# Performance work log

Hardware: AMD Instinct MI355X
Metric: run time of the kernel (lower is better)

The kernel has to match this reference:

```python
import jax, jax.numpy as jnp
import numpy as np

B, S, D = 4, 4096, 1024
E, I = 8, 2048
CAPACITY = 2
K = max(1, int(S / E * CAPACITY))  # tokens per expert per batch element


def setup_inputs() -> dict:
    key = jax.random.key(0)
    k1, k2, k3, k4, k5 = jax.random.split(key, 5)
    x = jax.random.normal(k1, (B, S, D), dtype=jnp.float32)
    gate_w = jax.random.normal(k2, (D, E), dtype=jnp.float32) * 0.006
    Wg = jax.random.normal(k3, (E, D, I), dtype=jnp.float32) * 0.02
    Wu = jax.random.normal(k4, (E, D, I), dtype=jnp.float32) * 0.02
    Wd = jax.random.normal(k5, (E, I, D), dtype=jnp.float32) * 0.02
    return {"x": x, "gate_w": gate_w, "Wg": Wg, "Wu": Wu, "Wd": Wd}


def reference(x, gate_w, Wg, Wu, Wd):
    # Router: softmax over experts per token, then per-expert top-k tokens.
    logits = jnp.einsum('bsd,de->bse', x, gate_w)          # [B,S,E]
    affinity = jax.nn.softmax(logits, axis=-1)
    affinity_T = jnp.transpose(affinity, (0, 2, 1))        # [B,E,S]
    gating, index = jax.lax.top_k(affinity_T, K)           # [B,E,K]

    # Gather selected tokens for all experts at once: [B,E,K,D]
    b_idx = jnp.arange(x.shape[0])[:, None, None]
    x_sel = x[b_idx, index]

    # Per-expert SwiGLU MLP (grouped GEMMs over the expert axis).
    g = jnp.einsum('bekd,edi->beki', x_sel, Wg)
    u = jnp.einsum('bekd,edi->beki', x_sel, Wu)
    h = jax.nn.silu(g) * u
    out = jnp.einsum('beki,eid->bekd', h, Wd)              # [B,E,K,D]

    # Weighted scatter-add combine back to token positions.
    contrib = out * gating[..., None]
    x_out = jnp.zeros_like(x).at[b_idx, index].add(contrib)
    return x_out
```

## Files before the change

kernel.cpp:

```cpp
#include <hip/hip_runtime.h>

#define B_ 4
#define S_ 4096
#define D_ 1024
#define E_ 8
#define I_ 2048
#define K_ 1024

typedef __attribute__((ext_vector_type(8))) short short8;
typedef __attribute__((ext_vector_type(4))) float f32x4;

__device__ __forceinline__ short f2bf(float f) {
  union { float f; unsigned u; } v; v.f = f;
  unsigned r = v.u + 0x7FFFu + ((v.u >> 16) & 1u);
  return (short)(r >> 16);
}

__device__ __forceinline__ void gload16(const void* g, void* l) {
  __builtin_amdgcn_global_load_lds((const __attribute__((address_space(1))) unsigned int*)g,
                                   (__attribute__((address_space(3))) unsigned int*)l, 16, 0, 0);
}

__device__ __forceinline__ short8 rdswz(const short* ls, int row, int cb) {
  int byte = (row << 7) + (cb ^ ((row & 7) << 4));
  return *reinterpret_cast<const short8*>(reinterpret_cast<const char*>(ls) + byte);
}

__global__ __launch_bounds__(256) void router_kernel(const float* __restrict__ x,
                                                     const float* __restrict__ gw,
                                                     double* __restrict__ affD) {
  int wave = threadIdx.x >> 6, lane = threadIdx.x & 63;
  int tok = blockIdx.x * 4 + wave;
  int b = tok >> 12, s = tok & (S_ - 1);
  const float* xr = x + (size_t)tok * D_;
  double acc[E_];
#pragma unroll
  for (int e = 0; e < E_; ++e) acc[e] = 0.0;
#pragma unroll 4
  for (int r = 0; r < 16; ++r) {
    int d = r * 64 + lane;
    float xv = xr[d];
    const float4* g4 = reinterpret_cast<const float4*>(gw + (size_t)d * E_);
    float4 g0 = g4[0], g1 = g4[1];
    acc[0] += (double)xv * g0.x; acc[1] += (double)xv * g0.y;
    acc[2] += (double)xv * g0.z; acc[3] += (double)xv * g0.w;
    acc[4] += (double)xv * g1.x; acc[5] += (double)xv * g1.y;
    acc[6] += (double)xv * g1.z; acc[7] += (double)xv * g1.w;
  }
#pragma unroll
  for (int off = 32; off > 0; off >>= 1) {
#pragma unroll
    for (int e = 0; e < E_; ++e) acc[e] += __shfl_xor(acc[e], off, 64);
  }
  double m = acc[0];
#pragma unroll
  for (int e = 1; e < E_; ++e) m = acc[e] > m ? acc[e] : m;
  double den = 0.0, ex[E_];
#pragma unroll
  for (int e = 0; e < E_; ++e) { ex[e] = exp(acc[e] - m); den += ex[e]; }
  if (lane < E_)
    affD[((size_t)b * E_ + lane) * S_ + s] = ex[lane] / den;
}

__global__ __launch_bounds__(1024) void topk_select_kernel(const double* __restrict__ affD,
                                                           int* __restrict__ idxArr,
                                                           float* __restrict__ gateArr) {
  __shared__ unsigned hist[256];
  __shared__ unsigned s_digit;
  __shared__ int s_rem;
  __shared__ unsigned s_cnt;
  int be = blockIdx.x, tid = threadIdx.x;
  const double* a = affD + (size_t)be * S_;
  unsigned long long key[4];
  bool active[4];
#pragma unroll
  for (int c = 0; c < 4; ++c) {
    int i = tid + c * 1024;
    unsigned long long kb = (unsigned long long)__double_as_longlong(a[i]);
    key[c] = (kb & ~0xFFFULL) | (unsigned long long)(4095 - i);
    active[c] = true;
  }
  int remk = K_;
  unsigned long long prefix = 0;
  for (int pass = 0; pass < 8; ++pass) {
    int shift = 56 - pass * 8;
    if (tid < 256) hist[tid] = 0;
    __syncthreads();
#pragma unroll
    for (int c = 0; c < 4; ++c)
      if (active[c]) atomicAdd(&hist[(unsigned)((key[c] >> shift) & 0xFF)], 1u);
    __syncthreads();
    if (tid == 0) {
      unsigned cum = 0; int d = 255;
      for (; d > 0; --d) {
        unsigned h = hist[d];
        if (cum + h >= (unsigned)remk) break;
        cum += h;
      }
      s_digit = (unsigned)d;
      s_rem = remk - (int)cum;
    }
    __syncthreads();
    unsigned dg = s_digit; remk = s_rem;
    prefix |= ((unsigned long long)dg) << shift;
#pragma unroll
    for (int c = 0; c < 4; ++c)
      active[c] = active[c] && (((key[c] >> shift) & 0xFF) == dg);
    __syncthreads();
  }
  if (tid == 0) s_cnt = 0;
  __syncthreads();
#pragma unroll
  for (int c = 0; c < 4; ++c) {
    if (key[c] >= prefix) {
      unsigned slot = atomicAdd(&s_cnt, 1u);
      int i = 4095 - (int)(key[c] & 0xFFF);
      idxArr[(size_t)be * K_ + slot] = i;
      gateArr[(size_t)be * K_ + slot] = (float)a[i];
    }
  }
}

__global__ __launch_bounds__(256) void transpose_cvt_kernel(const float* __restrict__ in,
                                                            unsigned short* __restrict__ out,
                                                            int M, int N) {
  __shared__ float t[64][65];
  int e = blockIdx.y;
  int ntn = N >> 6;
  int tm = (blockIdx.x / ntn) << 6;
  int tn = (blockIdx.x % ntn) << 6;
  const float* src = in + (size_t)e * M * N;
  unsigned short* dst = out + (size_t)e * M * N;
  int tid = threadIdx.x;
#pragma unroll
  for (int it = 0; it < 4; ++it) {
    int f = it * 256 + tid;
    int r = f >> 4, c4 = (f & 15) << 2;
    float4 v = *reinterpret_cast<const float4*>(&src[(size_t)(tm + r) * N + tn + c4]);
    t[c4][r] = v.x; t[c4 + 1][r] = v.y; t[c4 + 2][r] = v.z; t[c4 + 3][r] = v.w;
  }
  __syncthreads();
#pragma unroll
  for (int it = 0; it < 4; ++it) {
    int f = it * 256 + tid;
    int rr = f >> 4, c4 = (f & 15) << 2;
    short4 o;
    o.x = f2bf(t[rr][c4]); o.y = f2bf(t[rr][c4 + 1]);
    o.z = f2bf(t[rr][c4 + 2]); o.w = f2bf(t[rr][c4 + 3]);
    *reinterpret_cast<short4*>(&dst[(size_t)(tn + rr) * M + tm + c4]) = o;
  }
}

__global__ __launch_bounds__(256) void gather_cvt_kernel(const float* __restrict__ x,
                                                         const int* __restrict__ idxArr,
                                                         unsigned short* __restrict__ Xsel) {
  int row = blockIdx.x * 4 + (threadIdx.x >> 6);
  int lane = threadIdx.x & 63;
  int b = row >> 13;
  int tok = idxArr[row];
  const float* src = x + ((size_t)b * S_ + tok) * D_;
  unsigned short* dst = Xsel + (size_t)row * D_;
#pragma unroll
  for (int it = 0; it < 4; ++it) {
    int d = it * 256 + lane * 4;
    float4 v = *reinterpret_cast<const float4*>(src + d);
    short4 o;
    o.x = f2bf(v.x); o.y = f2bf(v.y); o.z = f2bf(v.z); o.w = f2bf(v.w);
    *reinterpret_cast<short4*>(dst + d) = o;
  }
}

__global__ __launch_bounds__(256, 2) void mlp1_kernel(
    const unsigned short* __restrict__ Xsel, const unsigned short* __restrict__ WgT,
    const unsigned short* __restrict__ WuT, unsigned short* __restrict__ H, int kc) {
  int nwg = gridDim.x;
  int bid = (blockIdx.x & 7) * (nwg >> 3) + (blockIdx.x >> 3);
  int nt = bid & 15; bid >>= 4;
  int mt = bid & 3; bid >>= 2;
  int be = bid;
  int e = be & 7;

  __shared__ short lsA[128 * 64];
  __shared__ short lsBg[128 * 64];
  __shared__ short lsBu[128 * 64];

  int tid = threadIdx.x, w = tid >> 6, lane = tid & 63;
  int wm = w >> 1, wn = w & 1;
  int lr = lane & 15, lg = lane >> 4;

  int srow = lane >> 3;
  int scol = ((lane & 7) ^ srow) << 4;

  const char* pa = (const char*)(Xsel + ((size_t)be * K_ + kc * 512 + mt * 128) * D_);
  const char* pg = (const char*)(WgT + ((size_t)e * I_ + nt * 128) * D_);
  const char* pu = (const char*)(WuT + ((size_t)e * I_ + nt * 128) * D_);

  f32x4 accg[4][4], accu[4][4];
#pragma unroll
  for (int i = 0; i < 4; ++i)
#pragma unroll
    for (int j = 0; j < 4; ++j) {
      accg[i][j] = (f32x4){0.f, 0.f, 0.f, 0.f};
      accu[i][j] = (f32x4){0.f, 0.f, 0.f, 0.f};
    }

  for (int k0 = 0; k0 < D_; k0 += 64) {
#pragma unroll
    for (int c = 0; c < 4; ++c) {
      int chunk = c * 4 + w;
      int row = chunk * 8 + srow;
      size_t go = (size_t)row * (D_ * 2) + (size_t)k0 * 2 + scol;
      gload16(pa + go, (char*)lsA + chunk * 1024);
      gload16(pg + go, (char*)lsBg + chunk * 1024);
      gload16(pu + go, (char*)lsBu + chunk * 1024);
    }
    __syncthreads();
#pragma unroll
    for (int fk = 0; fk < 2; ++fk) {
      int cb = fk * 64 + lg * 16;
      short8 af[4], bgf[4], buf[4];
#pragma unroll
      for (int fm = 0; fm < 4; ++fm)
        af[fm] = rdswz(lsA, wm * 64 + fm * 16 + lr, cb);
#pragma unroll
      for (int fn = 0; fn < 4; ++fn) {
        bgf[fn] = rdswz(lsBg, wn * 64 + fn * 16 + lr, cb);
        buf[fn] = rdswz(lsBu, wn * 64 + fn * 16 + lr, cb);
      }
#pragma unroll
      for (int fm = 0; fm < 4; ++fm)
#pragma unroll
        for (int fn = 0; fn < 4; ++fn) {
          accg[fm][fn] = __builtin_amdgcn_mfma_f32_16x16x32_bf16(af[fm], bgf[fn], accg[fm][fn], 0, 0, 0);
          accu[fm][fn] = __builtin_amdgcn_mfma_f32_16x16x32_bf16(af[fm], buf[fn], accu[fm][fn], 0, 0, 0);
        }
    }
    __syncthreads();
  }
  unsigned short* Hbe = H + (size_t)be * 512 * I_;
#pragma unroll
  for (int fm = 0; fm < 4; ++fm)
#pragma unroll
    for (int fn = 0; fn < 4; ++fn) {
#pragma unroll
      for (int j = 0; j < 4; ++j) {
        float g = accg[fm][fn][j], u = accu[fm][fn][j];
        float h = g / (1.f + __expf(-g)) * u;
        int row = wm * 64 + fm * 16 + lg * 4 + j;
        int col = wn * 64 + fn * 16 + lr;
        Hbe[(size_t)(mt * 128 + row) * I_ + nt * 128 + col] = (unsigned short)f2bf(h);
      }
    }
}

__global__ __launch_bounds__(256, 2) void mlp2_kernel(
    const unsigned short* __restrict__ H, const unsigned short* __restrict__ WdT,
    const int* __restrict__ idxArr, const float* __restrict__ gateArr,
    float* __restrict__ out, int kc) {
  int nwg = gridDim.x;
  int bid = (blockIdx.x & 7) * (nwg >> 3) + (blockIdx.x >> 3);
  int nt = bid & 7; bid >>= 3;
  int mt = bid & 3; bid >>= 2;
  int be = bid;
  int b = be >> 3, e = be & 7;

  __shared__ short lsA[128 * 64];
  __shared__ short lsB[128 * 64];
  __shared__ int sTok[128];
  __shared__ float sGate[128];

  int tid = threadIdx.x;
  if (tid < 128) {
    size_t gbase = (size_t)be * K_ + kc * 512 + mt * 128 + tid;
    sTok[tid] = idxArr[gbase];
    sGate[tid] = gateArr[gbase];
  }

  const char* pa = (const char*)(H + ((size_t)be * 512 + mt * 128) * I_);
  const char* pb = (const char*)(WdT + ((size_t)e * D_ + nt * 128) * I_);

  int w = tid >> 6, lane = tid & 63;
  int wm = w >> 1, wn = w & 1;
  int lr = lane & 15, lg = lane >> 4;

  int srow = lane >> 3;
  int scol = ((lane & 7) ^ srow) << 4;

  f32x4 acc[4][4];
#pragma unroll
  for (int i = 0; i < 4; ++i)
#pragma unroll
    for (int j = 0; j < 4; ++j) acc[i][j] = (f32x4){0.f, 0.f, 0.f, 0.f};

  for (int k0 = 0; k0 < I_; k0 += 64) {
#pragma unroll
    for (int c = 0; c < 4; ++c) {
      int chunk = c * 4 + w;
      int row = chunk * 8 + srow;
      size_t go = (size_t)row * (I_ * 2) + (size_t)k0 * 2 + scol;
      gload16(pa + go, (char*)lsA + chunk * 1024);
      gload16(pb + go, (char*)lsB + chunk * 1024);
    }
    __syncthreads();
#pragma unroll
    for (int fk = 0; fk < 2; ++fk) {
      int cb = fk * 64 + lg * 16;
      short8 af[4], bf[4];
#pragma unroll
      for (int fm = 0; fm < 4; ++fm)
        af[fm] = rdswz(lsA, wm * 64 + fm * 16 + lr, cb);
#pragma unroll
      for (int fn = 0; fn < 4; ++fn)
        bf[fn] = rdswz(lsB, wn * 64 + fn * 16 + lr, cb);
#pragma unroll
      for (int fm = 0; fm < 4; ++fm)
#pragma unroll
        for (int fn = 0; fn < 4; ++fn)
          acc[fm][fn] = __builtin_amdgcn_mfma_f32_16x16x32_bf16(af[fm], bf[fn], acc[fm][fn], 0, 0, 0);
    }
    __syncthreads();
  }
#pragma unroll
  for (int fm = 0; fm < 4; ++fm)
#pragma unroll
    for (int fn = 0; fn < 4; ++fn) {
#pragma unroll
      for (int j = 0; j < 4; ++j) {
        int row = wm * 64 + fm * 16 + lg * 4 + j;
        int col = nt * 128 + wn * 64 + fn * 16 + lr;
        float v = acc[fm][fn][j] * sGate[row];
        atomicAdd(&out[((size_t)b * S_ + sTok[row]) * D_ + col], v);
      }
    }
}

extern "C" void kernel_launch(void* const* d_in, const int* in_sizes, int n_in,
                              void* d_out, int out_size, void* d_ws, size_t ws_size,
                              hipStream_t stream) {
  const float* x  = (const float*)d_in[0];
  const float* gw = (const float*)d_in[1];
  const float* Wg = (const float*)d_in[2];
  const float* Wu = (const float*)d_in[3];
  const float* Wd = (const float*)d_in[4];
  float* out = (float*)d_out;
  char* ws = (char*)d_ws;

  size_t off = 0;
  double* affD = (double*)(ws + off); off += (size_t)B_ * E_ * S_ * sizeof(double);
  int* idxArr = (int*)(ws + off);     off += (size_t)B_ * E_ * K_ * sizeof(int);
  float* gateArr = (float*)(ws + off); off += (size_t)B_ * E_ * K_ * sizeof(float);
  off = (off + 255) & ~(size_t)255;
  unsigned short* WgT = (unsigned short*)(ws + off); off += (size_t)E_ * D_ * I_ * 2;
  unsigned short* WuT = (unsigned short*)(ws + off); off += (size_t)E_ * D_ * I_ * 2;
  unsigned short* WdT = (unsigned short*)(ws + off); off += (size_t)E_ * D_ * I_ * 2;
  unsigned short* Xsel = (unsigned short*)(ws + off); off += (size_t)B_ * E_ * K_ * D_ * 2;
  off = (off + 255) & ~(size_t)255;
  unsigned short* H = (unsigned short*)(ws + off);

  hipMemsetAsync(d_out, 0, (size_t)out_size * sizeof(float), stream);
  router_kernel<<<B_ * S_ / 4, 256, 0, stream>>>(x, gw, affD);
  topk_select_kernel<<<B_ * E_, 1024, 0, stream>>>(affD, idxArr, gateArr);
  transpose_cvt_kernel<<<dim3((D_ / 64) * (I_ / 64), E_), 256, 0, stream>>>(Wg, WgT, D_, I_);
  transpose_cvt_kernel<<<dim3((D_ / 64) * (I_ / 64), E_), 256, 0, stream>>>(Wu, WuT, D_, I_);
  transpose_cvt_kernel<<<dim3((I_ / 64) * (D_ / 64), E_), 256, 0, stream>>>(Wd, WdT, I_, D_);
  gather_cvt_kernel<<<B_ * E_ * K_ / 4, 256, 0, stream>>>(x, idxArr, Xsel);
  for (int kc = 0; kc < 2; ++kc) {
    mlp1_kernel<<<B_ * E_ * 4 * 16, 256, 0, stream>>>(Xsel, WgT, WuT, H, kc);
    mlp2_kernel<<<B_ * E_ * 4 * 8, 256, 0, stream>>>(H, WdT, idxArr, gateArr, out, kc);
  }
}
```

Baseline: 726.2 us.

## Widen mlp2 output tile to 128x256 and merge weight transpose launches

The down-projection GEMM now computes a 128x256 output tile per workgroup instead of 128x128. Each wave holds a 64x128 accumulator, which halves the grid and halves the number of times each H tile is re-read from memory. The three weight transpose/convert launches are merged into one launch whose grid y-dimension selects the weight matrix, removing two launch overheads. The wider tile doubles accumulator registers, which together with launch_bounds(256,2) risks spills or lower occupancy, and it raises LDS use for the B tile.

```diff
diff --git a/kernel.cpp b/kernel.cpp
--- a/kernel.cpp
+++ b/kernel.cpp
@@ -121,11 +121,19 @@
   }
 }
 
-__global__ __launch_bounds__(256) void transpose_cvt_kernel(const float* __restrict__ in,
-                                                            unsigned short* __restrict__ out,
-                                                            int M, int N) {
+__global__ __launch_bounds__(256) void transpose_cvt3_kernel(const float* __restrict__ Wg,
+                                                             const float* __restrict__ Wu,
+                                                             const float* __restrict__ Wd,
+                                                             unsigned short* __restrict__ WgT,
+                                                             unsigned short* __restrict__ WuT,
+                                                             unsigned short* __restrict__ WdT) {
   __shared__ float t[64][65];
-  int e = blockIdx.y;
+  int wsel = blockIdx.y >> 3;
+  int e = blockIdx.y & 7;
+  const float* in = wsel == 0 ? Wg : (wsel == 1 ? Wu : Wd);
+  unsigned short* out = wsel == 0 ? WgT : (wsel == 1 ? WuT : WdT);
+  int M = wsel == 2 ? I_ : D_;
+  int N = wsel == 2 ? D_ : I_;
   int ntn = N >> 6;
   int tm = (blockIdx.x / ntn) << 6;
   int tn = (blockIdx.x % ntn) << 6;
@@ -259,13 +267,13 @@
     float* __restrict__ out, int kc) {
   int nwg = gridDim.x;
   int bid = (blockIdx.x & 7) * (nwg >> 3) + (blockIdx.x >> 3);
-  int nt = bid & 7; bid >>= 3;
+  int nt = bid & 3; bid >>= 2;
   int mt = bid & 3; bid >>= 2;
   int be = bid;
   int b = be >> 3, e = be & 7;
 
   __shared__ short lsA[128 * 64];
-  __shared__ short lsB[128 * 64];
+  __shared__ short lsB[256 * 64];
   __shared__ int sTok[128];
   __shared__ float sGate[128];
 
@@ -277,7 +285,7 @@
   }
 
   const char* pa = (const char*)(H + ((size_t)be * 512 + mt * 128) * I_);
-  const char* pb = (const char*)(WdT + ((size_t)e * D_ + nt * 128) * I_);
+  const char* pb = (const char*)(WdT + ((size_t)e * D_ + nt * 256) * I_);
 
   int w = tid >> 6, lane = tid & 63;
   int wm = w >> 1, wn = w & 1;
@@ -286,36 +294,40 @@
   int srow = lane >> 3;
   int scol = ((lane & 7) ^ srow) << 4;
 
-  f32x4 acc[4][4];
+  f32x4 acc[4][8];
 #pragma unroll
   for (int i = 0; i < 4; ++i)
 #pragma unroll
-    for (int j = 0; j < 4; ++j) acc[i][j] = (f32x4){0.f, 0.f, 0.f, 0.f};
+    for (int j = 0; j < 8; ++j) acc[i][j] = (f32x4){0.f, 0.f, 0.f, 0.f};
 
   for (int k0 = 0; k0 < I_; k0 += 64) {
 #pragma unroll
     for (int c = 0; c < 4; ++c) {
       int chunk = c * 4 + w;
       int row = chunk * 8 + srow;
-      size_t go = (size_t)row * (I_ * 2) + (size_t)k0 * 2 + scol;
-      gload16(pa + go, (char*)lsA + chunk * 1024);
-      gload16(pb + go, (char*)lsB + chunk * 1024);
+      gload16(pa + (size_t)row * (I_ * 2) + (size_t)k0 * 2 + scol, (char*)lsA + chunk * 1024);
+    }
+#pragma unroll
+    for (int c = 0; c < 8; ++c) {
+      int chunk = c * 4 + w;
+      int row = chunk * 8 + srow;
+      gload16(pb + (size_t)row * (I_ * 2) + (size_t)k0 * 2 + scol, (char*)lsB + chunk * 1024);
     }
     __syncthreads();
 #pragma unroll
     for (int fk = 0; fk < 2; ++fk) {
       int cb = fk * 64 + lg * 16;
-      short8 af[4], bf[4];
+      short8 af[4], bf[8];
 #pragma unroll
       for (int fm = 0; fm < 4; ++fm)
         af[fm] = rdswz(lsA, wm * 64 + fm * 16 + lr, cb);
 #pragma unroll
-      for (int fn = 0; fn < 4; ++fn)
-        bf[fn] = rdswz(lsB, wn * 64 + fn * 16 + lr, cb);
+      for (int fn = 0; fn < 8; ++fn)
+        bf[fn] = rdswz(lsB, wn * 128 + fn * 16 + lr, cb);
 #pragma unroll
       for (int fm = 0; fm < 4; ++fm)
 #pragma unroll
-        for (int fn = 0; fn < 4; ++fn)
+        for (int fn = 0; fn < 8; ++fn)
           acc[fm][fn] = __builtin_amdgcn_mfma_f32_16x16x32_bf16(af[fm], bf[fn], acc[fm][fn], 0, 0, 0);
     }
     __syncthreads();
@@ -323,11 +335,11 @@
 #pragma unroll
   for (int fm = 0; fm < 4; ++fm)
 #pragma unroll
-    for (int fn = 0; fn < 4; ++fn) {
+    for (int fn = 0; fn < 8; ++fn) {
 #pragma unroll
       for (int j = 0; j < 4; ++j) {
         int row = wm * 64 + fm * 16 + lg * 4 + j;
-        int col = nt * 128 + wn * 64 + fn * 16 + lr;
+        int col = nt * 256 + wn * 128 + fn * 16 + lr;
         float v = acc[fm][fn][j] * sGate[row];
         atomicAdd(&out[((size_t)b * S_ + sTok[row]) * D_ + col], v);
       }
@@ -360,12 +372,11 @@
   hipMemsetAsync(d_out, 0, (size_t)out_size * sizeof(float), stream);
   router_kernel<<<B_ * S_ / 4, 256, 0, stream>>>(x, gw, affD);
   topk_select_kernel<<<B_ * E_, 1024, 0, stream>>>(affD, idxArr, gateArr);
-  transpose_cvt_kernel<<<dim3((D_ / 64) * (I_ / 64), E_), 256, 0, stream>>>(Wg, WgT, D_, I_);
-  transpose_cvt_kernel<<<dim3((D_ / 64) * (I_ / 64), E_), 256, 0, stream>>>(Wu, WuT, D_, I_);
-  transpose_cvt_kernel<<<dim3((I_ / 64) * (D_ / 64), E_), 256, 0, stream>>>(Wd, WdT, I_, D_);
+  transpose_cvt3_kernel<<<dim3((D_ / 64) * (I_ / 64), 3 * E_), 256, 0, stream>>>(
+      Wg, Wu, Wd, WgT, WuT, WdT);
   gather_cvt_kernel<<<B_ * E_ * K_ / 4, 256, 0, stream>>>(x, idxArr, Xsel);
   for (int kc = 0; kc < 2; ++kc) {
     mlp1_kernel<<<B_ * E_ * 4 * 16, 256, 0, stream>>>(Xsel, WgT, WuT, H, kc);
-    mlp2_kernel<<<B_ * E_ * 4 * 8, 256, 0, stream>>>(H, WdT, idxArr, gateArr, out, kc);
-  }
-}
+    mlp2_kernel<<<B_ * E_ * 4 * 4, 256, 0, stream>>>(H, WdT, idxArr, gateArr, out, kc);
+  }
+}
```

Result: no change. 713.0 us, median of 2 (-1.8%).
